# Kernel optimization log

Measured on AMD Instinct MI355X. Metric: run time of the kernel, lower is better.

## Reference

```python
import jax, jax.numpy as jnp
import numpy as np
import math

IN_FEATURES = 8192
OUT_FEATURES = 8192
IN_MODES = (32, 16, 16)   # balanced power-of-two split of 8192 over order 3
OUT_MODES = (32, 16, 16)
RANKS = (1, 4, 4, 1)
TOKENS = 128


def setup_inputs() -> dict:
    key = jax.random.key(0)
    k_in, k0, k1, k2, kb = jax.random.split(key, 5)
    inputs = jax.random.normal(k_in, (TOKENS, IN_FEATURES), dtype=jnp.float32)
    # cores: (left_rank, out_mode, in_mode, right_rank), init N(0, 0.02)
    core0 = 0.02 * jax.random.normal(k0, (RANKS[0], OUT_MODES[0], IN_MODES[0], RANKS[1]), dtype=jnp.float32)
    core1 = 0.02 * jax.random.normal(k1, (RANKS[1], OUT_MODES[1], IN_MODES[1], RANKS[2]), dtype=jnp.float32)
    core2 = 0.02 * jax.random.normal(k2, (RANKS[2], OUT_MODES[2], IN_MODES[2], RANKS[3]), dtype=jnp.float32)
    bound = 1.0 / math.sqrt(IN_FEATURES)
    bias = jax.random.uniform(kb, (OUT_FEATURES,), minval=-bound, maxval=bound, dtype=jnp.float32)
    return {"inputs": inputs, "core0": core0, "core1": core1, "core2": core2, "bias": bias}


def _dense_weight(core0, core1, core2):
    # chain contraction over TT ranks
    t = jnp.tensordot(core0, core1, axes=([-1], [0]))  # (1, o0, i0, o1, i1, r2)
    t = jnp.tensordot(t, core2, axes=([-1], [0]))      # (1, o0, i0, o1, i1, o2, i2, 1)
    t = jnp.squeeze(t, axis=(0, -1))                    # (o0, i0, o1, i1, o2, i2)
    # out modes first, then in modes (matches torch permute [0,2,4,1,3,5])
    t = jnp.transpose(t, (0, 2, 4, 1, 3, 5))
    w = t.reshape(math.prod(OUT_MODES), math.prod(IN_MODES))
    return w[:OUT_FEATURES, :IN_FEATURES]


def reference(inputs, core0, core1, core2, bias):
    weight = _dense_weight(core0, core1, core2)  # [out, in]
    return inputs @ weight.T + bias
```

## Files before the change

### kernel.cpp

```cpp
#include <hip/hip_runtime.h>


__device__ __forceinline__ void fma4(float4& a, float s, const float4& v) {
    a.x += s*v.x; a.y += s*v.y; a.z += s*v.z; a.w += s*v.w;
}
__device__ __forceinline__ float dot4(float4 a, float4 b) {
    return a.x*b.x + a.y*b.y + a.z*b.z + a.w*b.w;
}

__global__ __launch_bounds__(512, 4) void tt_fused(
    const float* __restrict__ x, const float* __restrict__ c0,
    const float* __restrict__ c1, const float* __restrict__ c2,
    const float* __restrict__ bias, float* __restrict__ out)
{
    __shared__ __align__(16) float smem[16384];
    float* y1s = smem;
    float* y2s = smem + 8192;
    float* pd  = smem;

    const int tid = threadIdx.x;
    const int b = blockIdx.x;
    const int t = b >> 2, q = b & 3;

    {
        const int i0 = tid >> 4, i1 = tid & 15;
        const float* xp = x + t*8192 + i0*256 + i1*16;
        const float4 x0 = *reinterpret_cast<const float4*>(xp + 0);
        const float4 x1 = *reinterpret_cast<const float4*>(xp + 4);
        const float4 x2 = *reinterpret_cast<const float4*>(xp + 8);
        const float4 x3 = *reinterpret_cast<const float4*>(xp + 12);
#pragma unroll
        for (int r2 = 0; r2 < 4; ++r2) {
            float s[4];
#pragma unroll
            for (int o2l = 0; o2l < 4; ++o2l) {
                const float4* cb =
                    reinterpret_cast<const float4*>(c2 + r2*256 + (q*4 + o2l)*16);
                s[o2l] = dot4(x0, cb[0]) + dot4(x1, cb[1])
                       + dot4(x2, cb[2]) + dot4(x3, cb[3]);
            }
            const int j = i1*4 + r2;
            *reinterpret_cast<float4*>(y1s + j*128 + ((i0 + j) & 31)*4) =
                make_float4(s[0], s[1], s[2], s[3]);
        }
    }
    __syncthreads();

    {
        const int o1 = tid >> 5, co = tid & 31;
        float4 acc0 = make_float4(0,0,0,0), acc1 = acc0, acc2 = acc0, acc3 = acc0;
        const float* c1p = c1 + o1*64;
#pragma unroll 2
        for (int jq = 0; jq < 16; ++jq) {
            const int j0 = jq*4;
            const float4 cv0 = *reinterpret_cast<const float4*>(c1p + 0*1024 + j0);
            const float4 cv1 = *reinterpret_cast<const float4*>(c1p + 1*1024 + j0);
            const float4 cv2 = *reinterpret_cast<const float4*>(c1p + 2*1024 + j0);
            const float4 cv3 = *reinterpret_cast<const float4*>(c1p + 3*1024 + j0);
            float4 yv[4];
#pragma unroll
            for (int jj = 0; jj < 4; ++jj) {
                const int j = j0 + jj;
                yv[jj] = *reinterpret_cast<const float4*>(y1s + j*128 + ((co + j) & 31)*4);
            }
            fma4(acc0, cv0.x, yv[0]); fma4(acc0, cv0.y, yv[1]);
            fma4(acc0, cv0.z, yv[2]); fma4(acc0, cv0.w, yv[3]);
            fma4(acc1, cv1.x, yv[0]); fma4(acc1, cv1.y, yv[1]);
            fma4(acc1, cv1.z, yv[2]); fma4(acc1, cv1.w, yv[3]);
            fma4(acc2, cv2.x, yv[0]); fma4(acc2, cv2.y, yv[1]);
            fma4(acc2, cv2.z, yv[2]); fma4(acc2, cv2.w, yv[3]);
            fma4(acc3, cv3.x, yv[0]); fma4(acc3, cv3.y, yv[1]);
            fma4(acc3, cv3.z, yv[2]); fma4(acc3, cv3.w, yv[3]);
        }
        *reinterpret_cast<float4*>(y2s + (co*4+0)*64 + ((o1 + co     ) & 15)*4) = acc0;
        *reinterpret_cast<float4*>(y2s + (co*4+1)*64 + ((o1 + co +  4) & 15)*4) = acc1;
        *reinterpret_cast<float4*>(y2s + (co*4+2)*64 + ((o1 + co +  8) & 15)*4) = acc2;
        *reinterpret_cast<float4*>(y2s + (co*4+3)*64 + ((o1 + co + 12) & 15)*4) = acc3;
    }
    __syncthreads();

    {
        const int ks = tid >> 7, o0q = (tid >> 4) & 7, colq = tid & 15;
        float4 acc[4];
#pragma unroll
        for (int m = 0; m < 4; ++m) acc[m] = make_float4(0,0,0,0);
        const float* c0p = c0 + o0q*4*128;
#pragma unroll 2
        for (int kq = 0; kq < 8; ++kq) {
            const int kb = ks*32 + kq*4;
            float4 yq[4];
#pragma unroll
            for (int kk = 0; kk < 4; ++kk) {
                const int k = kb + kk;
                const int phys = (colq + (k >> 2) + 4*(k & 3)) & 15;
                yq[kk] = *reinterpret_cast<const float4*>(y2s + k*64 + phys*4);
            }
            float4 cq[4];
#pragma unroll
            for (int o0l = 0; o0l < 4; ++o0l)
                cq[o0l] = *reinterpret_cast<const float4*>(c0p + o0l*128 + kb);
#pragma unroll
            for (int o0l = 0; o0l < 4; ++o0l) {
                fma4(acc[o0l], cq[o0l].x, yq[0]);
                fma4(acc[o0l], cq[o0l].y, yq[1]);
                fma4(acc[o0l], cq[o0l].z, yq[2]);
                fma4(acc[o0l], cq[o0l].w, yq[3]);
            }
        }
#pragma unroll
        for (int o0l = 0; o0l < 4; ++o0l)
            *reinterpret_cast<float4*>(pd + ks*2048 + (o0q*4 + o0l)*64 + colq*4) = acc[o0l];
    }
    __syncthreads();

    {
        const int o0 = tid >> 4, o1 = tid & 15;
        const float4 s0 = *reinterpret_cast<const float4*>(pd + 0    + o0*64 + o1*4);
        const float4 s1 = *reinterpret_cast<const float4*>(pd + 2048 + o0*64 + o1*4);
        const float4 s2 = *reinterpret_cast<const float4*>(pd + 4096 + o0*64 + o1*4);
        const float4 s3 = *reinterpret_cast<const float4*>(pd + 6144 + o0*64 + o1*4);
        const int ob = o0*256 + o1*16 + q*4;
        const float4 bq = *reinterpret_cast<const float4*>(bias + ob);
        *reinterpret_cast<float4*>(out + t*8192 + ob) =
            make_float4(s0.x+s1.x+s2.x+s3.x + bq.x,
                        s0.y+s1.y+s2.y+s3.y + bq.y,
                        s0.z+s1.z+s2.z+s3.z + bq.z,
                        s0.w+s1.w+s2.w+s3.w + bq.w);
    }
}

extern "C" void kernel_launch(void* const* d_in, const int* in_sizes, int n_in,
                              void* d_out, int out_size, void* d_ws, size_t ws_size,
                              hipStream_t stream) {
    const float* x    = (const float*)d_in[0];
    const float* c0   = (const float*)d_in[1];
    const float* c1   = (const float*)d_in[2];
    const float* c2   = (const float*)d_in[3];
    const float* bias = (const float*)d_in[4];
    float* out = (float*)d_out;
    (void)d_ws; (void)ws_size;

    tt_fused<<<512, 512, 0, stream>>>(x, c0, c1, c2, bias, out);
}
```

Baseline: 82.21 us.

## Stage core1 in LDS, pad y1 layout, use nontemporal x loads and output stores

Copies the 4096-float core1 tensor into shared memory at kernel start so the second contraction stage reads it from LDS instead of global/L1. Replaces the XOR-style swizzle of the y1 buffer with a padded row stride of 132 floats to avoid bank conflicts with simpler addressing. Loads of x and stores of the output become nontemporal to avoid polluting caches. Shared memory grows from 64KB to about 81KB per block, which may reduce blocks per CU.

```diff
diff --git a/kernel.cpp b/kernel.cpp
--- a/kernel.cpp
+++ b/kernel.cpp
@@ -1,10 +1,15 @@
 #include <hip/hip_runtime.h>
 
+
+typedef float v4f __attribute__((ext_vector_type(4)));
 
 __device__ __forceinline__ void fma4(float4& a, float s, const float4& v) {
     a.x += s*v.x; a.y += s*v.y; a.z += s*v.z; a.w += s*v.w;
 }
 __device__ __forceinline__ float dot4(float4 a, float4 b) {
+    return a.x*b.x + a.y*b.y + a.z*b.z + a.w*b.w;
+}
+__device__ __forceinline__ float dot4v(v4f a, float4 b) {
     return a.x*b.x + a.y*b.y + a.z*b.z + a.w*b.w;
 }
 
@@ -13,9 +18,10 @@
     const float* __restrict__ c1, const float* __restrict__ c2,
     const float* __restrict__ bias, float* __restrict__ out)
 {
-    __shared__ __align__(16) float smem[16384];
+    __shared__ __align__(16) float smem[20736];
     float* y1s = smem;
-    float* y2s = smem + 8192;
+    float* y2s = smem + 8448;
+    float* c1s = smem + 16640;
     float* pd  = smem;
 
     const int tid = threadIdx.x;
@@ -23,12 +29,20 @@
     const int t = b >> 2, q = b & 3;
 
     {
+        const int f = tid * 8;
+        const float4 a0 = *reinterpret_cast<const float4*>(c1 + f);
+        const float4 a1 = *reinterpret_cast<const float4*>(c1 + f + 4);
+        *reinterpret_cast<float4*>(c1s + f)     = a0;
+        *reinterpret_cast<float4*>(c1s + f + 4) = a1;
+    }
+
+    {
         const int i0 = tid >> 4, i1 = tid & 15;
         const float* xp = x + t*8192 + i0*256 + i1*16;
-        const float4 x0 = *reinterpret_cast<const float4*>(xp + 0);
-        const float4 x1 = *reinterpret_cast<const float4*>(xp + 4);
-        const float4 x2 = *reinterpret_cast<const float4*>(xp + 8);
-        const float4 x3 = *reinterpret_cast<const float4*>(xp + 12);
+        const v4f x0 = __builtin_nontemporal_load(reinterpret_cast<const v4f*>(xp + 0));
+        const v4f x1 = __builtin_nontemporal_load(reinterpret_cast<const v4f*>(xp + 4));
+        const v4f x2 = __builtin_nontemporal_load(reinterpret_cast<const v4f*>(xp + 8));
+        const v4f x3 = __builtin_nontemporal_load(reinterpret_cast<const v4f*>(xp + 12));
 #pragma unroll
         for (int r2 = 0; r2 < 4; ++r2) {
             float s[4];
@@ -36,11 +50,11 @@
             for (int o2l = 0; o2l < 4; ++o2l) {
                 const float4* cb =
                     reinterpret_cast<const float4*>(c2 + r2*256 + (q*4 + o2l)*16);
-                s[o2l] = dot4(x0, cb[0]) + dot4(x1, cb[1])
-                       + dot4(x2, cb[2]) + dot4(x3, cb[3]);
+                s[o2l] = dot4v(x0, cb[0]) + dot4v(x1, cb[1])
+                       + dot4v(x2, cb[2]) + dot4v(x3, cb[3]);
             }
             const int j = i1*4 + r2;
-            *reinterpret_cast<float4*>(y1s + j*128 + ((i0 + j) & 31)*4) =
+            *reinterpret_cast<float4*>(y1s + j*132 + i0*4) =
                 make_float4(s[0], s[1], s[2], s[3]);
         }
     }
@@ -49,7 +63,8 @@
     {
         const int o1 = tid >> 5, co = tid & 31;
         float4 acc0 = make_float4(0,0,0,0), acc1 = acc0, acc2 = acc0, acc3 = acc0;
-        const float* c1p = c1 + o1*64;
+        const float* c1p = c1s + o1*64;
+        const float* y1p = y1s + co*4;
 #pragma unroll 2
         for (int jq = 0; jq < 16; ++jq) {
             const int j0 = jq*4;
@@ -59,10 +74,8 @@
             const float4 cv3 = *reinterpret_cast<const float4*>(c1p + 3*1024 + j0);
             float4 yv[4];
 #pragma unroll
-            for (int jj = 0; jj < 4; ++jj) {
-                const int j = j0 + jj;
-                yv[jj] = *reinterpret_cast<const float4*>(y1s + j*128 + ((co + j) & 31)*4);
-            }
+            for (int jj = 0; jj < 4; ++jj)
+                yv[jj] = *reinterpret_cast<const float4*>(y1p + (j0 + jj)*132);
             fma4(acc0, cv0.x, yv[0]); fma4(acc0, cv0.y, yv[1]);
             fma4(acc0, cv0.z, yv[2]); fma4(acc0, cv0.w, yv[3]);
             fma4(acc1, cv1.x, yv[0]); fma4(acc1, cv1.y, yv[1]);
@@ -121,11 +134,11 @@
         const float4 s3 = *reinterpret_cast<const float4*>(pd + 6144 + o0*64 + o1*4);
         const int ob = o0*256 + o1*16 + q*4;
         const float4 bq = *reinterpret_cast<const float4*>(bias + ob);
-        *reinterpret_cast<float4*>(out + t*8192 + ob) =
-            make_float4(s0.x+s1.x+s2.x+s3.x + bq.x,
+        const v4f r = { s0.x+s1.x+s2.x+s3.x + bq.x,
                         s0.y+s1.y+s2.y+s3.y + bq.y,
                         s0.z+s1.z+s2.z+s3.z + bq.z,
-                        s0.w+s1.w+s2.w+s3.w + bq.w);
+                        s0.w+s1.w+s2.w+s3.w + bq.w };
+        __builtin_nontemporal_store(r, reinterpret_cast<v4f*>(out + t*8192 + ob));
     }
 }
 
```

Measured after the change: 87.48 us. 6.4% more time.
